# Kernel optimization log

Measured on AMD Instinct MI355X. Metric: run time of the kernel, lower is better.

The kernel has to match this reference:

```python
import jax, jax.numpy as jnp
import numpy as np

N, S, H = 16, 2048, 1024
K = 8           # num_models (experts)
D = H // 4      # bottleneck = hidden_dim // ds_factor


def setup_inputs() -> dict:
    key = jax.random.key(0)
    k1, k2, k3, k4, k5, k6 = jax.random.split(key, 6)
    hidden_states = jax.random.normal(k1, (N, S, H), dtype=jnp.float32)
    p = jax.random.uniform(k2, (N, K), dtype=jnp.float32)
    prob = p / jnp.sum(p, axis=-1, keepdims=True)  # normalized routing probs
    std = 0.02
    w_down = jax.random.normal(k3, (K, D, H), dtype=jnp.float32) * std
    b_down = jax.random.normal(k4, (K, D), dtype=jnp.float32) * std
    w_up = jax.random.normal(k5, (K, H, D), dtype=jnp.float32) * std
    b_up = jax.random.normal(k6, (K, H), dtype=jnp.float32) * std
    return {"hidden_states": hidden_states, "prob": prob,
            "w_down": w_down, "b_down": b_down,
            "w_up": w_up, "b_up": b_up}


def merge_linear(x, prob, weight, bias):
    # weight: (K, out, in); prob: (N, K) -> per-instance merged weight (N, out, in)
    w = jnp.einsum('nk,koi->noi', prob, weight)
    b = jnp.einsum('nk,ko->no', prob, bias)
    # x: (N, S, in) -> (N, S, out); matmul with per-instance weight^T
    y = jnp.einsum('nsi,noi->nso', x, w)
    return y + b[:, None, :]


def reference(hidden_states, prob, w_down, b_down, w_up, b_up):
    # MergeAdapter forward (ln_before=False, ln_after=False, dropout=0)
    residual = merge_linear(hidden_states, prob, w_down, b_down)
    residual = jax.nn.relu(residual)
    residual = merge_linear(residual, prob, w_up, b_up)
    return hidden_states + residual
```

## Files before the change

kernel.cpp:

```cpp
#include <hip/hip_runtime.h>


typedef unsigned short u16;
typedef __bf16 bf16x8 __attribute__((ext_vector_type(8)));
typedef float f32x4 __attribute__((ext_vector_type(4)));

__device__ __forceinline__ u16 f2bf(float f) {
    union { float f; unsigned int i; } v; v.f = f;
    unsigned int r = v.i + 0x7fffu + ((v.i >> 16) & 1u);
    return (u16)(r >> 16);
}

__device__ __forceinline__ void gload_lds16(const u16* g, u16* l) {
    __builtin_amdgcn_global_load_lds(
        (const __attribute__((address_space(1))) void*)g,
        (__attribute__((address_space(3))) void*)l,
        16, 0, 0);
}

__global__ __launch_bounds__(256)
void merge_kernel(const float* __restrict__ prob,
                  const float* __restrict__ w_down, const float* __restrict__ b_down,
                  const float* __restrict__ w_up,   const float* __restrict__ b_up,
                  u16* __restrict__ Wd, u16* __restrict__ Wu,
                  float* __restrict__ bd, float* __restrict__ bu)
{
    __shared__ float sp[128];
    const int tid = threadIdx.x;
    if (tid < 128) sp[tid] = prob[tid];
    __syncthreads();

    const int bid = blockIdx.x;
    const int E = 256 * 1024;

    if (bid < 256) {
        int v = bid * 256 + tid;
        const bool down = (v < 32768);
        const int vv = down ? v : (v - 32768);
        const float* W = down ? w_down : w_up;
        u16* O = down ? Wd : Wu;
        const size_t e = (size_t)vv * 8;

        float wf[8][8];
        #pragma unroll
        for (int k = 0; k < 8; ++k) {
            const float4 f0 = *(const float4*)(W + (size_t)k * E + e);
            const float4 f1 = *(const float4*)(W + (size_t)k * E + e + 4);
            wf[k][0] = f0.x; wf[k][1] = f0.y; wf[k][2] = f0.z; wf[k][3] = f0.w;
            wf[k][4] = f1.x; wf[k][5] = f1.y; wf[k][6] = f1.z; wf[k][7] = f1.w;
        }
        for (int n = 0; n < 16; ++n) {
            float a[8] = {0.f,0.f,0.f,0.f,0.f,0.f,0.f,0.f};
            #pragma unroll
            for (int k = 0; k < 8; ++k) {
                const float p = sp[n * 8 + k];
                #pragma unroll
                for (int j = 0; j < 8; ++j) a[j] = fmaf(p, wf[k][j], a[j]);
            }
            union { uint4 u; u16 s[8]; } ov;
            #pragma unroll
            for (int j = 0; j < 8; ++j) ov.s[j] = f2bf(a[j]);
            *(uint4*)(O + (size_t)n * E + e) = ov.u;
        }
    } else {
        int idx = (bid - 256) * 256 + tid;
        if (idx < 16 * 256) {
            const int n = idx >> 8, d = idx & 255;
            float s = 0.f;
            #pragma unroll
            for (int k = 0; k < 8; ++k)
                s = fmaf(sp[n * 8 + k], b_down[k * 256 + d], s);
            bd[idx] = s;
        } else {
            const int i2 = idx - 4096;
            const int n = i2 >> 10, h = i2 & 1023;
            float s = 0.f;
            #pragma unroll
            for (int k = 0; k < 8; ++k)
                s = fmaf(sp[n * 8 + k], b_up[k * 1024 + h], s);
            bu[i2] = s;
        }
    }
}

__global__ __launch_bounds__(512, 1)
void fused_adapter(const float* __restrict__ x, const u16* __restrict__ Wd,
                   const u16* __restrict__ Wu, const float* __restrict__ bd,
                   const float* __restrict__ bu, float* __restrict__ out)
{
    __shared__ __align__(16) u16 Rs[128 * 256];
    __shared__ __align__(16) u16 stage[32768];

    const int tid  = threadIdx.x;
    const int lane = tid & 63;
    const int wave = tid >> 6;
    const int quad = lane >> 4, rl = lane & 15;

    const int id = blockIdx.x;
    const int r4 = id & 15;
    const int batch = (r4 & 7) * 2 + (r4 >> 3);
    const int mblk  = id >> 4;

    const float* xb  = x  + (size_t)batch * 2048 * 1024 + (size_t)mblk * 128 * 1024;
    const u16*   Wdb = Wd + (size_t)batch * 256 * 1024;
    const u16*   Wub = Wu + (size_t)batch * 1024 * 256;
    const float* bdb = bd + batch * 256;
    const float* bub = bu + batch * 1024;
    float*       ob  = out + (size_t)batch * 2048 * 1024 + (size_t)mblk * 128 * 1024;

    u16* xs  = stage;
    u16* wds = stage + 8192;

    const int wm1 = wave >> 2, wn1 = wave & 3;
    f32x4 acc1[4][4] = {};

    for (int k0 = 0; k0 < 1024; k0 += 64) {
        #pragma unroll
        for (int rr = 0; rr < 4; ++rr) {
            const int li  = rr * 512 + tid;
            const int row = li >> 3, col = (li & 7) * 8;
            gload_lds16(Wdb + (size_t)row * 1024 + (k0 + col),
                        wds + (size_t)(rr * 512 + wave * 64) * 8);
        }
        #pragma unroll
        for (int rr = 0; rr < 2; ++rr) {
            const int li  = rr * 512 + tid;
            const int row = li >> 3, col = (li & 7) * 8;
            const float4 f0 = *(const float4*)(xb + (size_t)row * 1024 + (k0 + col));
            const float4 f1 = *(const float4*)(xb + (size_t)row * 1024 + (k0 + col) + 4);
            union { uint4 u; u16 s[8]; } cv;
            cv.s[0]=f2bf(f0.x); cv.s[1]=f2bf(f0.y); cv.s[2]=f2bf(f0.z); cv.s[3]=f2bf(f0.w);
            cv.s[4]=f2bf(f1.x); cv.s[5]=f2bf(f1.y); cv.s[6]=f2bf(f1.z); cv.s[7]=f2bf(f1.w);
            *(uint4*)(xs + (size_t)li * 8) = cv.u;
        }
        __syncthreads();

        #pragma unroll
        for (int kk = 0; kk < 64; kk += 32) {
            bf16x8 af[4], bfv[4];
            #pragma unroll
            for (int mi = 0; mi < 4; ++mi)
                af[mi] = *(const bf16x8*)(xs + (wm1 * 64 + mi * 16 + rl) * 64 + kk + quad * 8);
            #pragma unroll
            for (int ni = 0; ni < 4; ++ni)
                bfv[ni] = *(const bf16x8*)(wds + (wn1 * 64 + ni * 16 + rl) * 64 + kk + quad * 8);
            #pragma unroll
            for (int mi = 0; mi < 4; ++mi)
                #pragma unroll
                for (int ni = 0; ni < 4; ++ni)
                    acc1[mi][ni] = __builtin_amdgcn_mfma_f32_16x16x32_bf16(
                        af[mi], bfv[ni], acc1[mi][ni], 0, 0, 0);
        }
        __syncthreads();
    }

    #pragma unroll
    for (int ni = 0; ni < 4; ++ni) {
        const int col = wn1 * 64 + ni * 16 + rl;
        const float bv = bdb[col];
        #pragma unroll
        for (int mi = 0; mi < 4; ++mi) {
            #pragma unroll
            for (int i = 0; i < 4; ++i) {
                const int row = wm1 * 64 + mi * 16 + quad * 4 + i;
                Rs[row * 256 + col] = f2bf(fmaxf(acc1[mi][ni][i] + bv, 0.0f));
            }
        }
    }

    const int wm2 = wave >> 2, wn2 = wave & 3;

    for (int c = 0; c < 8; ++c) {
        __syncthreads();

        #pragma unroll
        for (int rr = 0; rr < 8; ++rr) {
            const int li  = rr * 512 + tid;
            const int row = li >> 5, col = (li & 31) * 8;
            gload_lds16(Wub + (size_t)(c * 128 + row) * 256 + col,
                        stage + (size_t)(rr * 512 + wave * 64) * 8);
        }
        __syncthreads();

        f32x4 acc2[4][2] = {};
        #pragma unroll
        for (int kk = 0; kk < 256; kk += 32) {
            bf16x8 af[4], bfv[2];
            #pragma unroll
            for (int mi = 0; mi < 4; ++mi)
                af[mi] = *(const bf16x8*)(Rs + (wm2 * 64 + mi * 16 + rl) * 256 + kk + quad * 8);
            #pragma unroll
            for (int ni = 0; ni < 2; ++ni)
                bfv[ni] = *(const bf16x8*)(stage + (wn2 * 32 + ni * 16 + rl) * 256 + kk + quad * 8);
            #pragma unroll
            for (int mi = 0; mi < 4; ++mi)
                #pragma unroll
                for (int ni = 0; ni < 2; ++ni)
                    acc2[mi][ni] = __builtin_amdgcn_mfma_f32_16x16x32_bf16(
                        af[mi], bfv[ni], acc2[mi][ni], 0, 0, 0);
        }

        #pragma unroll
        for (int ni = 0; ni < 2; ++ni) {
            const int colg = c * 128 + wn2 * 32 + ni * 16 + rl;
            const float bv = bub[colg];
            #pragma unroll
            for (int mi = 0; mi < 4; ++mi) {
                #pragma unroll
                for (int i = 0; i < 4; ++i) {
                    const int rowl = wm2 * 64 + mi * 16 + quad * 4 + i;
                    const size_t off = (size_t)rowl * 1024 + colg;
                    ob[off] = acc2[mi][ni][i] + bv + xb[off];
                }
            }
        }
    }
}

extern "C" void kernel_launch(void* const* d_in, const int* in_sizes, int n_in,
                              void* d_out, int out_size, void* d_ws, size_t ws_size,
                              hipStream_t stream) {
    const float* hidden = (const float*)d_in[0];
    const float* prob   = (const float*)d_in[1];
    const float* w_down = (const float*)d_in[2];
    const float* b_down = (const float*)d_in[3];
    const float* w_up   = (const float*)d_in[4];
    const float* b_up   = (const float*)d_in[5];
    float* out = (float*)d_out;

    u16* Wd = (u16*)d_ws;
    u16* Wu = Wd + (size_t)16 * 256 * 1024;
    float* bd = (float*)(Wu + (size_t)16 * 1024 * 256);
    float* bu = bd + 16 * 256;

    merge_kernel<<<336, 256, 0, stream>>>(prob, w_down, b_down, w_up, b_up,
                                          Wd, Wu, bd, bu);

    fused_adapter<<<256, 512, 0, stream>>>(hidden, Wd, Wu, bd, bu, out);
}
```

Measured before the change: 331.7 us.

## Double-buffer both GEMM stages with XOR-swizzled LDS and register-resident activations

```diff
diff --git a/kernel.cpp b/kernel.cpp
--- a/kernel.cpp
+++ b/kernel.cpp
@@ -16,6 +16,13 @@
         (const __attribute__((address_space(1))) void*)g,
         (__attribute__((address_space(3))) void*)l,
         16, 0, 0);
+}
+
+__device__ __forceinline__ void store8(u16* dst, float4 a, float4 b) {
+    union { uint4 u; u16 s[8]; } cv;
+    cv.s[0]=f2bf(a.x); cv.s[1]=f2bf(a.y); cv.s[2]=f2bf(a.z); cv.s[3]=f2bf(a.w);
+    cv.s[4]=f2bf(b.x); cv.s[5]=f2bf(b.y); cv.s[6]=f2bf(b.z); cv.s[7]=f2bf(b.w);
+    *(uint4*)dst = cv.u;
 }
 
 __global__ __launch_bounds__(256)
@@ -83,18 +90,19 @@
     }
 }
 
-__global__ __launch_bounds__(512, 1)
+__global__ __launch_bounds__(512, 2)
 void fused_adapter(const float* __restrict__ x, const u16* __restrict__ Wd,
                    const u16* __restrict__ Wu, const float* __restrict__ bd,
                    const float* __restrict__ bu, float* __restrict__ out)
 {
-    __shared__ __align__(16) u16 Rs[128 * 256];
-    __shared__ __align__(16) u16 stage[32768];
+    __shared__ __align__(16) u16 lds0[32768];
+    __shared__ __align__(16) u16 lds1[32768];
 
     const int tid  = threadIdx.x;
     const int lane = tid & 63;
     const int wave = tid >> 6;
     const int quad = lane >> 4, rl = lane & 15;
+    const int rxl  = rl & 7;
 
     const int id = blockIdx.x;
     const int r4 = id & 15;
@@ -108,49 +116,72 @@
     const float* bub = bu + batch * 1024;
     float*       ob  = out + (size_t)batch * 2048 * 1024 + (size_t)mblk * 128 * 1024;
 
-    u16* xs  = stage;
-    u16* wds = stage + 8192;
-
     const int wm1 = wave >> 2, wn1 = wave & 3;
+
+    u16* const b0x = lds1;  u16* const b0w = lds1 + 8192;
+    u16* const b1x = lds0;  u16* const b1w = lds0 + 8192;
+
+    const int xrow = tid >> 3, xsl = tid & 7;
+    const int xdst0 = (xrow * 8 + (xsl ^ (xrow & 7))) * 8;
+    const int xdst1 = xdst0 + 4096;
+    const int wrow  = tid >> 3;
+    const int wgcol = ((tid & 7) ^ ((tid >> 3) & 7)) * 8;
+
     f32x4 acc1[4][4] = {};
 
-    for (int k0 = 0; k0 < 1024; k0 += 64) {
-        #pragma unroll
-        for (int rr = 0; rr < 4; ++rr) {
-            const int li  = rr * 512 + tid;
-            const int row = li >> 3, col = (li & 7) * 8;
-            gload_lds16(Wdb + (size_t)row * 1024 + (k0 + col),
-                        wds + (size_t)(rr * 512 + wave * 64) * 8);
-        }
-        #pragma unroll
-        for (int rr = 0; rr < 2; ++rr) {
-            const int li  = rr * 512 + tid;
-            const int row = li >> 3, col = (li & 7) * 8;
-            const float4 f0 = *(const float4*)(xb + (size_t)row * 1024 + (k0 + col));
-            const float4 f1 = *(const float4*)(xb + (size_t)row * 1024 + (k0 + col) + 4);
-            union { uint4 u; u16 s[8]; } cv;
-            cv.s[0]=f2bf(f0.x); cv.s[1]=f2bf(f0.y); cv.s[2]=f2bf(f0.z); cv.s[3]=f2bf(f0.w);
-            cv.s[4]=f2bf(f1.x); cv.s[5]=f2bf(f1.y); cv.s[6]=f2bf(f1.z); cv.s[7]=f2bf(f1.w);
-            *(uint4*)(xs + (size_t)li * 8) = cv.u;
-        }
-        __syncthreads();
+    {
+        const float4 a0 = *(const float4*)(xb + (size_t)xrow * 1024 + xsl * 8);
+        const float4 a1 = *(const float4*)(xb + (size_t)xrow * 1024 + xsl * 8 + 4);
+        const float4 a2 = *(const float4*)(xb + (size_t)(xrow + 64) * 1024 + xsl * 8);
+        const float4 a3 = *(const float4*)(xb + (size_t)(xrow + 64) * 1024 + xsl * 8 + 4);
+        #pragma unroll
+        for (int r = 0; r < 4; ++r)
+            gload_lds16(Wdb + (size_t)(r * 64 + wrow) * 1024 + wgcol,
+                        b0w + (size_t)(r * 512 + wave * 64) * 8);
+        store8(b0x + xdst0, a0, a1);
+        store8(b0x + xdst1, a2, a3);
+    }
+    __syncthreads();
+
+    for (int it = 0; it < 16; ++it) {
+        u16* cx = (it & 1) ? b1x : b0x;
+        u16* cw = (it & 1) ? b1w : b0w;
+        u16* nx = (it & 1) ? b0x : b1x;
+        u16* nw = (it & 1) ? b0w : b1w;
+        const int k1 = (it + 1) * 64;
+
+        float4 a0, a1, a2, a3;
+        if (it < 15) {
+            a0 = *(const float4*)(xb + (size_t)xrow * 1024 + k1 + xsl * 8);
+            a1 = *(const float4*)(xb + (size_t)xrow * 1024 + k1 + xsl * 8 + 4);
+            a2 = *(const float4*)(xb + (size_t)(xrow + 64) * 1024 + k1 + xsl * 8);
+            a3 = *(const float4*)(xb + (size_t)(xrow + 64) * 1024 + k1 + xsl * 8 + 4);
+            #pragma unroll
+            for (int r = 0; r < 4; ++r)
+                gload_lds16(Wdb + (size_t)(r * 64 + wrow) * 1024 + k1 + wgcol,
+                            nw + (size_t)(r * 512 + wave * 64) * 8);
+        }
 
         #pragma unroll
         for (int kk = 0; kk < 64; kk += 32) {
-            bf16x8 af[4], bfv[4];
-            #pragma unroll
-            for (int mi = 0; mi < 4; ++mi)
-                af[mi] = *(const bf16x8*)(xs + (wm1 * 64 + mi * 16 + rl) * 64 + kk + quad * 8);
+            bf16x8 av[4], bv[4];
+            #pragma unroll
+            for (int mi = 0; mi < 4; ++mi)
+                av[mi] = *(const bf16x8*)(cx + (wm1 * 64 + mi * 16 + rl) * 64
+                                          + ((kk / 8 + quad) ^ rxl) * 8);
             #pragma unroll
             for (int ni = 0; ni < 4; ++ni)
-                bfv[ni] = *(const bf16x8*)(wds + (wn1 * 64 + ni * 16 + rl) * 64 + kk + quad * 8);
+                bv[ni] = *(const bf16x8*)(cw + (wn1 * 64 + ni * 16 + rl) * 64
+                                          + ((kk / 8 + quad) ^ rxl) * 8);
             #pragma unroll
             for (int mi = 0; mi < 4; ++mi)
                 #pragma unroll
                 for (int ni = 0; ni < 4; ++ni)
                     acc1[mi][ni] = __builtin_amdgcn_mfma_f32_16x16x32_bf16(
-                        af[mi], bfv[ni], acc1[mi][ni], 0, 0, 0);
-        }
+                        av[mi], bv[ni], acc1[mi][ni], 0, 0, 0);
+        }
+
+        if (it < 15) { store8(nx + xdst0, a0, a1); store8(nx + xdst1, a2, a3); }
         __syncthreads();
     }
 
@@ -158,46 +189,68 @@
     for (int ni = 0; ni < 4; ++ni) {
         const int col = wn1 * 64 + ni * 16 + rl;
         const float bv = bdb[col];
-        #pragma unroll
-        for (int mi = 0; mi < 4; ++mi) {
+        const int lbc = col >> 3, hi = lbc & 24, c7 = lbc & 7, cl = col & 7;
+        #pragma unroll
+        for (int mi = 0; mi < 4; ++mi)
             #pragma unroll
             for (int i = 0; i < 4; ++i) {
                 const int row = wm1 * 64 + mi * 16 + quad * 4 + i;
-                Rs[row * 256 + col] = f2bf(fmaxf(acc1[mi][ni][i] + bv, 0.0f));
+                const int phys = hi | (c7 ^ (row & 7));
+                lds0[row * 256 + phys * 8 + cl] =
+                    f2bf(fmaxf(acc1[mi][ni][i] + bv, 0.0f));
             }
-        }
-    }
+    }
+    __syncthreads();
 
     const int wm2 = wave >> 2, wn2 = wave & 3;
 
+    const int srow = tid >> 5, ss = tid & 31;
+    const int wugcol = ((ss & 24) | ((ss & 7) ^ (srow & 7))) * 8;
+
+    auto stage_wu = [&](int c, u16* buf) {
+        #pragma unroll
+        for (int rr = 0; rr < 8; ++rr)
+            gload_lds16(Wub + (size_t)(c * 128 + rr * 16 + srow) * 256 + wugcol,
+                        buf + (size_t)(rr * 512 + wave * 64) * 8);
+    };
+
+    stage_wu(0, lds1);
+
+    bf16x8 af[4][8];
+    #pragma unroll
+    for (int mi = 0; mi < 4; ++mi) {
+        const int rowb = (wm2 * 64 + mi * 16 + rl) * 256;
+        #pragma unroll
+        for (int t = 0; t < 8; ++t) {
+            const int lb = t * 4 + quad;
+            const int phys = (lb & 24) | ((lb & 7) ^ rxl);
+            af[mi][t] = *(const bf16x8*)(lds0 + rowb + phys * 8);
+        }
+    }
+    __syncthreads();
+
+    u16* cur = lds1;
+    u16* nxt = lds0;
     for (int c = 0; c < 8; ++c) {
-        __syncthreads();
-
-        #pragma unroll
-        for (int rr = 0; rr < 8; ++rr) {
-            const int li  = rr * 512 + tid;
-            const int row = li >> 5, col = (li & 31) * 8;
-            gload_lds16(Wub + (size_t)(c * 128 + row) * 256 + col,
-                        stage + (size_t)(rr * 512 + wave * 64) * 8);
-        }
-        __syncthreads();
+        if (c < 7) stage_wu(c + 1, nxt);
 
         f32x4 acc2[4][2] = {};
         #pragma unroll
-        for (int kk = 0; kk < 256; kk += 32) {
-            bf16x8 af[4], bfv[2];
-            #pragma unroll
-            for (int mi = 0; mi < 4; ++mi)
-                af[mi] = *(const bf16x8*)(Rs + (wm2 * 64 + mi * 16 + rl) * 256 + kk + quad * 8);
-            #pragma unroll
-            for (int ni = 0; ni < 2; ++ni)
-                bfv[ni] = *(const bf16x8*)(stage + (wn2 * 32 + ni * 16 + rl) * 256 + kk + quad * 8);
+        for (int t = 0; t < 8; ++t) {
+            bf16x8 bv[2];
+            #pragma unroll
+            for (int ni = 0; ni < 2; ++ni) {
+                const int rowb = (wn2 * 32 + ni * 16 + rl) * 256;
+                const int lb = t * 4 + quad;
+                const int phys = (lb & 24) | ((lb & 7) ^ rxl);
+                bv[ni] = *(const bf16x8*)(cur + rowb + phys * 8);
+            }
             #pragma unroll
             for (int mi = 0; mi < 4; ++mi)
                 #pragma unroll
                 for (int ni = 0; ni < 2; ++ni)
                     acc2[mi][ni] = __builtin_amdgcn_mfma_f32_16x16x32_bf16(
-                        af[mi], bfv[ni], acc2[mi][ni], 0, 0, 0);
+                        af[mi][t], bv[ni], acc2[mi][ni], 0, 0, 0);
         }
 
         #pragma unroll
@@ -205,14 +258,18 @@
             const int colg = c * 128 + wn2 * 32 + ni * 16 + rl;
             const float bv = bub[colg];
             #pragma unroll
-            for (int mi = 0; mi < 4; ++mi) {
+            for (int mi = 0; mi < 4; ++mi)
                 #pragma unroll
                 for (int i = 0; i < 4; ++i) {
                     const int rowl = wm2 * 64 + mi * 16 + quad * 4 + i;
                     const size_t off = (size_t)rowl * 1024 + colg;
                     ob[off] = acc2[mi][ni][i] + bv + xb[off];
                 }
-            }
+        }
+
+        if (c < 7) {
+            u16* t2 = cur; cur = nxt; nxt = t2;
+            __syncthreads();
         }
     }
 }
```

Result: no change. 329.0 us (-0.8%).
